# Optimization experiments

Measured on AMD Instinct MI355X. Metric: run time of the kernel, lower is better.

## Reference

```python
import jax, jax.numpy as jnp
import numpy as np

K = 7  # local_kernel_size


def conv2d(x, w, b, pad):
    # x: [B,C,H,W], w: [O,I,kh,kw]
    y = jax.lax.conv_general_dilated(
        x, w, window_strides=(1, 1), padding=[(pad, pad), (pad, pad)],
        dimension_numbers=("NCHW", "OIHW", "NCHW"))
    return y + b[None, :, None, None]


def kernel_normalize(kernel, k):
    # kernel: [B, k*k, H, W]; zero-mean over tap dim, then add 1/(k*k)
    km = jnp.mean(kernel, axis=1, keepdims=True)
    return kernel - km + 1.0 / (k * k)


def local_conv_feat(img, kernel, k):
    # Fused dynamic local conv: avoids materializing [B,C,k*k,H,W].
    # Tap order matches F.unfold row-major (dy, dx).
    B, C, H, W = img.shape
    pad = (k - 1) // 2
    imgp = jnp.pad(img, ((0, 0), (0, 0), (pad, pad), (pad, pad)))
    out = jnp.zeros_like(img)
    for dy in range(k):
        for dx in range(k):
            idx = dy * k + dx
            out = out + imgp[:, :, dy:dy + H, dx:dx + W] * kernel[:, idx:idx + 1]
    return out


def setup_inputs() -> dict:
    key = jax.random.key(0)
    ks = jax.random.split(key, 14)
    B, C, H, W = 4, 64, 128, 128
    w = lambda k, shape: jax.random.normal(k, shape, jnp.float32) * 0.05
    return {
        "x": jax.random.normal(ks[0], (B, C, H, W), jnp.float32),
        "kernel_features": jax.random.normal(ks[1], (B, C, H, W), jnp.float32),
        # feature_path: two 3x3 convs
        "fw1": w(ks[2], (C, C, 3, 3)), "fb1": jnp.zeros((C,), jnp.float32),
        "fw2": w(ks[3], (C, C, 3, 3)), "fb2": jnp.zeros((C,), jnp.float32),
        # multiplicative_path: two 3x3 convs
        "mw1": w(ks[4], (C, C, 3, 3)), "mb1": jnp.zeros((C,), jnp.float32),
        "mw2": w(ks[5], (C, C, 3, 3)), "mb2": jnp.zeros((C,), jnp.float32),
        # local_filter_path: two 1x1 convs, last outputs k*k channels
        "lw1": w(ks[6], (C, C, 1, 1)), "lb1": jnp.zeros((C,), jnp.float32),
        "lw2": w(ks[7], (K * K, C, 1, 1)), "lb2": jnp.zeros((K * K,), jnp.float32),
    }


def reference(x, kernel_features, fw1, fb1, fw2, fb2, mw1, mb1, mw2, mb2, lw1, lb1, lw2, lb2):
    # feature_path: ReLU -> conv3x3 -> ReLU -> conv3x3
    fp = conv2d(jax.nn.relu(conv2d(jax.nn.relu(x), fw1, fb1, 1)), fw2, fb2, 1)
    # multiplicative_path: conv3x3 -> ReLU -> conv3x3
    mp = conv2d(jax.nn.relu(conv2d(kernel_features, mw1, mb1, 1)), mw2, mb2, 1)
    # local_filter_path: conv1x1 -> ReLU -> conv1x1 (-> k*k channels)
    lp = conv2d(jax.nn.relu(conv2d(kernel_features, lw1, lb1, 0)), lw2, lb2, 0)
    lp = kernel_normalize(lp, K)
    feat = fp * mp
    filtered = local_conv_feat(feat, lp, K)
    return x + filtered
```

## Files before the change

### kernel.cpp

```cpp
#include <hip/hip_runtime.h>
#include <hip/hip_bf16.h>

#define Cc 64
#define Hc 128
#define Wc 128
#define HWc (Hc * Wc)
#define Bc 4

typedef __attribute__((ext_vector_type(8))) short short8;
typedef __attribute__((ext_vector_type(4))) float float4v;

static __device__ __forceinline__ unsigned short f2bu(float f) {
    __hip_bfloat16 h = __float2bfloat16(f);
    return *(unsigned short*)&h;
}

__global__ __launch_bounds__(256) void cvt_both_k(
    const float* __restrict__ x, const float* __restrict__ kf,
    unsigned short* __restrict__ xb, unsigned short* __restrict__ kfb)
{
    const int bid = blockIdx.x;
    const bool isx = bid < 256;
    const float* src = isx ? x : kf;
    unsigned short* dst = isx ? xb : kfb;
    const int px = (isx ? bid : bid - 256) * 256 + threadIdx.x;
    const int b  = px >> 14;
    const int hw = px & 16383;
    const float* s = src + (size_t)b * Cc * HWc + hw;
    unsigned short* d = dst + (size_t)px * Cc;

#pragma unroll
    for (int c8 = 0; c8 < 8; ++c8) {
        unsigned int pk[4];
#pragma unroll
        for (int jp = 0; jp < 4; ++jp) {
            float v0 = s[(size_t)(c8 * 8 + jp * 2 + 0) * HWc];
            float v1 = s[(size_t)(c8 * 8 + jp * 2 + 1) * HWc];
            if (isx) { v0 = fmaxf(v0, 0.f); v1 = fmaxf(v1, 0.f); }
            pk[jp] = (unsigned int)f2bu(v0) | ((unsigned int)f2bu(v1) << 16);
        }
        *(uint4*)(d + c8 * 8) = make_uint4(pk[0], pk[1], pk[2], pk[3]);
    }
}

__global__ __launch_bounds__(256) void wpack_all_k(
    const float* __restrict__ fw1, const float* __restrict__ fw2,
    const float* __restrict__ mw1, const float* __restrict__ mw2,
    const float* __restrict__ lw1, const float* __restrict__ lw2,
    unsigned short* __restrict__ wbase)
{
    const int bid = blockIdx.x;
    const int tid = threadIdx.x;
    if (bid < 72) {
        const int which = bid / 18;
        const float* w = (which == 0) ? fw1 : (which == 1) ? fw2 : (which == 2) ? mw1 : mw2;
        unsigned short* wb = wbase + (size_t)which * 36864;
        const int g = (bid % 18) * 256 + tid;
        if (g >= 4608) return;
        const int lane = g & 63;
        const int smt  = g >> 6;
        const int s    = smt >> 2;
        const int mt   = smt & 3;
        const int co   = mt * 16 + (lane & 15);
        const int kb   = s * 32 + (lane >> 4) * 8;
        unsigned int pk[4];
#pragma unroll
        for (int jp = 0; jp < 4; ++jp) {
            int k0 = kb + jp * 2, k1 = k0 + 1;
            float v0 = w[((size_t)co * Cc + (k0 & 63)) * 9 + (k0 >> 6)];
            float v1 = w[((size_t)co * Cc + (k1 & 63)) * 9 + (k1 >> 6)];
            pk[jp] = (unsigned int)f2bu(v0) | ((unsigned int)f2bu(v1) << 16);
        }
        *(uint4*)(wb + (size_t)g * 8) = make_uint4(pk[0], pk[1], pk[2], pk[3]);
    } else {
        const int which = (bid - 72) >> 1;
        const float* w = which ? lw2 : lw1;
        const int Cout = which ? 49 : 64;
        unsigned short* wb = wbase + 4 * 36864 + (size_t)which * 4096;
        const int g = ((bid - 72) & 1) * 256 + tid;
        const int lane = g & 63;
        const int smt  = g >> 6;
        const int s    = smt >> 2;
        const int mt   = smt & 3;
        const int co   = mt * 16 + (lane & 15);
        const int kb   = s * 32 + (lane >> 4) * 8;
        unsigned int pk[4];
#pragma unroll
        for (int jp = 0; jp < 4; ++jp) {
            int k0 = kb + jp * 2, k1 = k0 + 1;
            float v0 = (co < Cout) ? w[(size_t)co * Cc + k0] : 0.f;
            float v1 = (co < Cout) ? w[(size_t)co * Cc + k1] : 0.f;
            pk[jp] = (unsigned int)f2bu(v0) | ((unsigned int)f2bu(v1) << 16);
        }
        *(uint4*)(wb + (size_t)g * 8) = make_uint4(pk[0], pk[1], pk[2], pk[3]);
    }
}

#define STAGE_TILE(INPTR)                                                     \
    for (int u = tid; u < 264; u += 256) {                                    \
        const int r_  = u / 66;                                               \
        const int c_  = u - r_ * 66;                                          \
        const int gh_ = h0 - 1 + r_;                                          \
        const int gw_ = w0 - 1 + c_;                                          \
        const bool ok_ = ((unsigned)gh_ < (unsigned)Hc) && ((unsigned)gw_ < (unsigned)Wc); \
        const unsigned short* src_ =                                          \
            (INPTR) + (((size_t)b * Hc + (ok_ ? gh_ : 0)) * Wc + (ok_ ? gw_ : 0)) * Cc; \
        const int sw_ = u & 7;                                                \
        _Pragma("unroll")                                                     \
        for (int ch_ = 0; ch_ < 8; ++ch_) {                                   \
            uint4 v_ = ok_ ? *(const uint4*)(src_ + ch_ * 8) : make_uint4(0, 0, 0, 0); \
            *(uint4*)&s_b[u * 64 + ((ch_ ^ sw_) << 3)] = v_;                  \
        }                                                                     \
    }

#define LOAD_A(W, s, m) (*(const short8*)((W) + (size_t)(s) * 2048 + (size_t)(m) * 512))
#define LOAD_B(s, nt) ({                                                      \
        const int tap_ = (s) >> 1;                                            \
        const int qb_  = rowb[tap_ / 3] + tap_ % 3;                           \
        const int ch0_ = ((s) & 1) * 4 + quad;                                \
        *(const short8*)&s_b[(qb_ + (nt) * 16) * 64 + ((ch0_ ^ (qb_ & 7)) << 3)]; })

#define CONV_GEMM(APTR, ACC)                                                  \
    {                                                                         \
        short8 a_cur[2], b_cur[4];                                            \
        _Pragma("unroll")                                                     \
        for (int m = 0; m < 2; ++m) a_cur[m] = LOAD_A(APTR, 0, m);            \
        _Pragma("unroll")                                                     \
        for (int nt = 0; nt < 4; ++nt) b_cur[nt] = LOAD_B(0, nt);             \
        _Pragma("unroll")                                                     \
        for (int s = 0; s < 18; ++s) {                                        \
            short8 a_nxt[2], b_nxt[4];                                        \
            if (s < 17) {                                                     \
                _Pragma("unroll")                                             \
                for (int m = 0; m < 2; ++m) a_nxt[m] = LOAD_A(APTR, s + 1, m);\
                _Pragma("unroll")                                             \
                for (int nt = 0; nt < 4; ++nt) b_nxt[nt] = LOAD_B(s + 1, nt); \
            }                                                                 \
            _Pragma("unroll")                                                 \
            for (int nt = 0; nt < 4; ++nt)                                    \
                _Pragma("unroll")                                             \
                for (int m = 0; m < 2; ++m)                                   \
                    ACC[m][nt] = __builtin_amdgcn_mfma_f32_16x16x32_bf16(     \
                        a_cur[m], b_cur[nt], ACC[m][nt], 0, 0, 0);            \
            if (s < 17) {                                                     \
                _Pragma("unroll")                                             \
                for (int m = 0; m < 2; ++m) a_cur[m] = a_nxt[m];              \
                _Pragma("unroll")                                             \
                for (int nt = 0; nt < 4; ++nt) b_cur[nt] = b_nxt[nt];         \
            }                                                                 \
        }                                                                     \
    }

__global__ __launch_bounds__(256) void conv1_dual_k(
    const unsigned short* __restrict__ in0,
    const unsigned short* __restrict__ in1,
    const unsigned short* __restrict__ wfrag0,
    const unsigned short* __restrict__ wfrag1,
    const float* __restrict__ bias0,
    const float* __restrict__ bias1,
    unsigned short* __restrict__ out0,
    unsigned short* __restrict__ out1)
{
    __shared__ unsigned short s_b[264 * 64];

    const int tid  = threadIdx.x;
    const int lane = tid & 63;
    const int wv   = tid >> 6;
    const int w0   = blockIdx.x * 64;
    const int h0   = blockIdx.y * 2;
    const int zz   = blockIdx.z;
    const int b    = zz & 3;
    const bool sel = zz >> 2;

    const unsigned short* in    = sel ? in1 : in0;
    const unsigned short* wfrag = sel ? wfrag1 : wfrag0;
    const float*          bias  = sel ? bias1 : bias0;
    unsigned short*       out   = sel ? out1 : out0;

    STAGE_TILE(in);
    __syncthreads();

    const int rowsel = wv >> 1;
    const int cohalf = wv & 1;
    const int quad   = lane >> 4;
    const int n15    = lane & 15;
    const unsigned short* aptr = wfrag + (((size_t)(cohalf * 2) * 64 + lane) << 3);

    int rowb[3];
#pragma unroll
    for (int ky = 0; ky < 3; ++ky) rowb[ky] = (rowsel + ky) * 66 + n15;

    float4v acc[2][4];
#pragma unroll
    for (int m = 0; m < 2; ++m)
#pragma unroll
        for (int nt = 0; nt < 4; ++nt) acc[m][nt] = (float4v){0.f, 0.f, 0.f, 0.f};

    CONV_GEMM(aptr, acc);

    const int h = h0 + rowsel;
#pragma unroll
    for (int m = 0; m < 2; ++m) {
        const int mt  = cohalf * 2 + m;
        const int co0 = mt * 16 + quad * 4;
        float4 bv = *(const float4*)&bias[co0];
#pragma unroll
        for (int nt = 0; nt < 4; ++nt) {
            const size_t pix = ((size_t)b * Hc + h) * Wc + w0 + nt * 16 + n15;
            ushort4 pk;
            pk.x = f2bu(fmaxf(acc[m][nt][0] + bv.x, 0.f));
            pk.y = f2bu(fmaxf(acc[m][nt][1] + bv.y, 0.f));
            pk.z = f2bu(fmaxf(acc[m][nt][2] + bv.z, 0.f));
            pk.w = f2bu(fmaxf(acc[m][nt][3] + bv.w, 0.f));
            *(ushort4*)&out[pix * Cc + co0] = pk;
        }
    }
}

__global__ __launch_bounds__(256) void conv2_fused_k(
    const unsigned short* __restrict__ t1f,
    const unsigned short* __restrict__ t1m,
    const unsigned short* __restrict__ wf,
    const unsigned short* __restrict__ wm,
    const float* __restrict__ bf,
    const float* __restrict__ bm,
    float* __restrict__ feat)
{
    __shared__ unsigned short s_b[264 * 64];

    const int tid  = threadIdx.x;
    const int lane = tid & 63;
    const int wv   = tid >> 6;
    const int w0   = blockIdx.x * 64;
    const int h0   = blockIdx.y * 2;
    const int b    = blockIdx.z;

    const int rowsel = wv >> 1;
    const int cohalf = wv & 1;
    const int quad   = lane >> 4;
    const int n15    = lane & 15;

    int rowb[3];
#pragma unroll
    for (int ky = 0; ky < 3; ++ky) rowb[ky] = (rowsel + ky) * 66 + n15;

    STAGE_TILE(t1f);
    __syncthreads();

    float4v acc[2][4];
#pragma unroll
    for (int m = 0; m < 2; ++m)
#pragma unroll
        for (int nt = 0; nt < 4; ++nt) acc[m][nt] = (float4v){0.f, 0.f, 0.f, 0.f};

    {
        const unsigned short* aptr = wf + (((size_t)(cohalf * 2) * 64 + lane) << 3);
        CONV_GEMM(aptr, acc);
    }

    unsigned int fpk[2][4][2];
#pragma unroll
    for (int m = 0; m < 2; ++m) {
        const int mt  = cohalf * 2 + m;
        const int co0 = mt * 16 + quad * 4;
        float4 bv = *(const float4*)&bf[co0];
#pragma unroll
        for (int nt = 0; nt < 4; ++nt) {
            fpk[m][nt][0] = (unsigned int)f2bu(acc[m][nt][0] + bv.x)
                          | ((unsigned int)f2bu(acc[m][nt][1] + bv.y) << 16);
            fpk[m][nt][1] = (unsigned int)f2bu(acc[m][nt][2] + bv.z)
                          | ((unsigned int)f2bu(acc[m][nt][3] + bv.w) << 16);
        }
    }

    __syncthreads();

    STAGE_TILE(t1m);
    __syncthreads();

#pragma unroll
    for (int m = 0; m < 2; ++m)
#pragma unroll
        for (int nt = 0; nt < 4; ++nt) acc[m][nt] = (float4v){0.f, 0.f, 0.f, 0.f};

    {
        const unsigned short* aptr = wm + (((size_t)(cohalf * 2) * 64 + lane) << 3);
        CONV_GEMM(aptr, acc);
    }

    const int h = h0 + rowsel;
#pragma unroll
    for (int m = 0; m < 2; ++m) {
        const int mt  = cohalf * 2 + m;
        const int co0 = mt * 16 + quad * 4;
        float4 bv = *(const float4*)&bm[co0];
#pragma unroll
        for (int nt = 0; nt < 4; ++nt) {
            float v[4] = {acc[m][nt][0] + bv.x, acc[m][nt][1] + bv.y,
                          acc[m][nt][2] + bv.z, acc[m][nt][3] + bv.w};
            v[0] *= __uint_as_float((fpk[m][nt][0] & 0xffffu) << 16);
            v[1] *= __uint_as_float(fpk[m][nt][0] & 0xffff0000u);
            v[2] *= __uint_as_float((fpk[m][nt][1] & 0xffffu) << 16);
            v[3] *= __uint_as_float(fpk[m][nt][1] & 0xffff0000u);
#pragma unroll
            for (int r = 0; r < 4; ++r)
                feat[((size_t)b * Cc + co0 + r) * HWc + (size_t)h * Wc + w0 + nt * 16 + n15] = v[r];
        }
    }
}

__global__ __launch_bounds__(256) void lp_fused_k(
    const unsigned short* __restrict__ in,
    const unsigned short* __restrict__ w1,
    const float* __restrict__ b1,
    const unsigned short* __restrict__ w2,
    const float* __restrict__ b2,
    float* __restrict__ out)
{
    __shared__ unsigned short s_t[4 * 1024];

    const int tid  = threadIdx.x;
    const int lane = tid & 63;
    const int wv   = tid >> 6;
    const int quad = lane >> 4;
    const int p    = lane & 15;
    const size_t pix = (size_t)blockIdx.x * 64 + wv * 16 + p;
    unsigned short* st = &s_t[wv * 1024];

    float4v acc1[4];
#pragma unroll
    for (int mt = 0; mt < 4; ++mt) acc1[mt] = (float4v){0.f, 0.f, 0.f, 0.f};
#pragma unroll
    for (int s = 0; s < 2; ++s) {
        short8 bfr = *(const short8*)&in[pix * Cc + s * 32 + quad * 8];
#pragma unroll
        for (int mt = 0; mt < 4; ++mt) {
            short8 afr = *(const short8*)&w1[(size_t)(((s * 4 + mt) << 6) + lane) << 3];
            acc1[mt] = __builtin_amdgcn_mfma_f32_16x16x32_bf16(afr, bfr, acc1[mt], 0, 0, 0);
        }
    }

#pragma unroll
    for (int mt = 0; mt < 4; ++mt) {
        const int co0 = mt * 16 + quad * 4;
        float4 bv = *(const float4*)&b1[co0];
        ushort4 pk;
        pk.x = f2bu(fmaxf(acc1[mt][0] + bv.x, 0.f));
        pk.y = f2bu(fmaxf(acc1[mt][1] + bv.y, 0.f));
        pk.z = f2bu(fmaxf(acc1[mt][2] + bv.z, 0.f));
        pk.w = f2bu(fmaxf(acc1[mt][3] + bv.w, 0.f));
        const int cg = co0 >> 3;
        *(ushort4*)&st[p * 64 + ((cg ^ (p & 7)) << 3) + (quad & 1) * 4] = pk;
    }
    __syncthreads();

    float4v acc2[4];
#pragma unroll
    for (int mt = 0; mt < 4; ++mt) acc2[mt] = (float4v){0.f, 0.f, 0.f, 0.f};
#pragma unroll
    for (int s = 0; s < 2; ++s) {
        const int cg = s * 4 + quad;
        short8 bfr = *(const short8*)&st[p * 64 + ((cg ^ (p & 7)) << 3)];
#pragma unroll
        for (int mt = 0; mt < 4; ++mt) {
            short8 afr = *(const short8*)&w2[(size_t)(((s * 4 + mt) << 6) + lane) << 3];
            acc2[mt] = __builtin_amdgcn_mfma_f32_16x16x32_bf16(afr, bfr, acc2[mt], 0, 0, 0);
        }
    }

    float v[4][4];
    float partial = 0.f;
#pragma unroll
    for (int mt = 0; mt < 4; ++mt) {
#pragma unroll
        for (int r = 0; r < 4; ++r) {
            const int tap = mt * 16 + quad * 4 + r;
            float val = (tap < 49) ? (acc2[mt][r] + b2[tap]) : 0.f;
            v[mt][r] = val;
            partial += val;
        }
    }
    partial += __shfl_xor(partial, 16, 64);
    partial += __shfl_xor(partial, 32, 64);
    const float m = partial * (1.f / 49.f) - (1.f / 49.f);

    const int b  = (int)(pix >> 14);
    const int hw = (int)(pix & 16383);
#pragma unroll
    for (int mt = 0; mt < 4; ++mt) {
#pragma unroll
        for (int r = 0; r < 4; ++r) {
            const int tap = mt * 16 + quad * 4 + r;
            if (tap < 49)
                out[((size_t)b * 49 + tap) * HWc + hw] = v[mt][r] - m;
        }
    }
}

__global__ __launch_bounds__(256) void local_conv_v2(
    const float* __restrict__ x, const float* __restrict__ feat,
    const float* __restrict__ lp, float* __restrict__ out)
{
    const int tid = threadIdx.x;
    const int w4  = (tid & 31) * 4;
    const int ro  = tid >> 5;
    const int h   = blockIdx.y * 8 + ro;
    const int c0  = blockIdx.x * 4;
    const int b   = blockIdx.z;

    float msk[12];
#pragma unroll
    for (int e = 0; e < 12; ++e) {
        int gw = w4 - 4 + e;
        msk[e] = ((unsigned)gw < (unsigned)Wc) ? 1.f : 0.f;
    }

    float acc[4][4];
#pragma unroll
    for (int ch = 0; ch < 4; ++ch)
#pragma unroll
        for (int p = 0; p < 4; ++p) acc[ch][p] = 0.f;

    const float* lpb = lp + (size_t)b * 49 * HWc + (size_t)h * Wc + w4;
    const float* fb  = feat + ((size_t)b * Cc + c0) * HWc;

#pragma unroll
    for (int dy = 0; dy < 7; ++dy) {
        const int gh = h + dy - 3;
        if ((unsigned)gh >= (unsigned)Hc) continue;

        float4 lp4[7];
#pragma unroll
        for (int dx = 0; dx < 7; ++dx)
            lp4[dx] = *(const float4*)&lpb[(size_t)(dy * 7 + dx) * HWc];

        const float* frow = fb + (size_t)gh * Wc + w4;
#pragma unroll
        for (int ch = 0; ch < 4; ++ch) {
            const float* fr = frow + (size_t)ch * HWc;
            float4 a  = *(const float4*)(fr - 4);
            float4 bq = *(const float4*)(fr);
            float4 cq = *(const float4*)(fr + 4);
            float f[12];
            f[0]  = a.x;            f[1]  = a.y * msk[1];
            f[2]  = a.z * msk[2];   f[3]  = a.w * msk[3];
            f[4]  = bq.x;           f[5]  = bq.y;
            f[6]  = bq.z;           f[7]  = bq.w;
            f[8]  = cq.x * msk[8];  f[9]  = cq.y * msk[9];
            f[10] = cq.z * msk[10]; f[11] = cq.w;
#pragma unroll
            for (int dx = 0; dx < 7; ++dx) {
                const float* lpv = (const float*)&lp4[dx];
#pragma unroll
                for (int p = 0; p < 4; ++p)
                    acc[ch][p] = fmaf(f[p + dx + 1], lpv[p], acc[ch][p]);
            }
        }
    }

#pragma unroll
    for (int ch = 0; ch < 4; ++ch) {
        const size_t idx = ((size_t)b * Cc + c0 + ch) * HWc + (size_t)h * Wc + w4;
        float4 xv = *(const float4*)&x[idx];
        float4 r  = {acc[ch][0] + xv.x, acc[ch][1] + xv.y,
                     acc[ch][2] + xv.z, acc[ch][3] + xv.w};
        *(float4*)&out[idx] = r;
    }
}

extern "C" void kernel_launch(void* const* d_in, const int* in_sizes, int n_in,
                              void* d_out, int out_size, void* d_ws, size_t ws_size,
                              hipStream_t stream)
{
    const float* x   = (const float*)d_in[0];
    const float* kf  = (const float*)d_in[1];
    const float* fw1 = (const float*)d_in[2];
    const float* fb1 = (const float*)d_in[3];
    const float* fw2 = (const float*)d_in[4];
    const float* fb2 = (const float*)d_in[5];
    const float* mw1 = (const float*)d_in[6];
    const float* mb1 = (const float*)d_in[7];
    const float* mw2 = (const float*)d_in[8];
    const float* mb2 = (const float*)d_in[9];
    const float* lw1 = (const float*)d_in[10];
    const float* lb1 = (const float*)d_in[11];
    const float* lw2 = (const float*)d_in[12];
    const float* lb2 = (const float*)d_in[13];

    float* out = (float*)d_out;
    char*  ws  = (char*)d_ws;

    const size_t NBH = (size_t)Bc * HWc * Cc * 2;
    const size_t NBF = (size_t)Bc * Cc * HWc * 4;
    const size_t LPB = (size_t)Bc * 49 * HWc * 4;

    unsigned short* t1f   = (unsigned short*)(ws);
    unsigned short* t1m   = (unsigned short*)(ws + NBH);
    float*          feat  = (float*)(ws + 2 * NBH);
    float*          lpb   = (float*)(ws + 2 * NBH + NBF);
    unsigned short* xb    = (unsigned short*)(ws + 2 * NBH + NBF + LPB);
    unsigned short* kfb   = (unsigned short*)((char*)xb + NBH);
    unsigned short* wbase = (unsigned short*)((char*)kfb + NBH);
    unsigned short* wb1   = wbase;
    unsigned short* wb2   = wbase + 36864;
    unsigned short* wb3   = wbase + 2 * 36864;
    unsigned short* wb4   = wbase + 3 * 36864;
    unsigned short* wl1   = wbase + 4 * 36864;
    unsigned short* wl2   = wbase + 4 * 36864 + 4096;

    dim3 blk(256);
    dim3 gm2(Wc / 64, Hc / 2, Bc * 2);
    dim3 gm (Wc / 64, Hc / 2, Bc);
    dim3 gp (Bc * HWc / 64);
    dim3 glc(Cc / 4, Hc / 8, Bc);

    cvt_both_k<<<dim3(512), blk, 0, stream>>>(x, kf, xb, kfb);
    wpack_all_k<<<dim3(76), blk, 0, stream>>>(fw1, fw2, mw1, mw2, lw1, lw2, wbase);

    conv1_dual_k<<<gm2, blk, 0, stream>>>(xb, kfb, wb1, wb3, fb1, mb1, t1f, t1m);

    conv2_fused_k<<<gm, blk, 0, stream>>>(t1f, t1m, wb2, wb4, fb2, mb2, feat);

    lp_fused_k<<<gp, blk, 0, stream>>>(kfb, wl1, lb1, wl2, lb2, lpb);

    local_conv_v2<<<glc, blk, 0, stream>>>(x, feat, lpb, out);
}
```

Baseline: 192.0 us.

## Stage conv tiles via global_load_lds DMA, double-buffer conv2 inputs, merge prep kernels

Replaces the register-staged halo tile loads in both conv kernels with direct global-to-LDS loads (global_load_lds), using a zeroed page for out-of-bounds pixels. conv2 now stages both input tiles up front into two LDS buffers, which removes the mid-kernel barrier and restage. The conversion and weight-packing kernels are merged into one launch. The cost is double the LDS in conv2, which may lower occupancy, plus an extra memset.

```diff
diff --git a/kernel.cpp b/kernel.cpp
--- a/kernel.cpp
+++ b/kernel.cpp
@@ -15,47 +15,50 @@
     return *(unsigned short*)&h;
 }
 
-__global__ __launch_bounds__(256) void cvt_both_k(
+static __device__ __forceinline__ void gl_lds16(const void* g, void* l) {
+    __builtin_amdgcn_global_load_lds(
+        (const __attribute__((address_space(1))) unsigned int*)g,
+        (__attribute__((address_space(3))) unsigned int*)l, 16, 0, 0);
+}
+
+__global__ __launch_bounds__(256) void prep_k(
     const float* __restrict__ x, const float* __restrict__ kf,
-    unsigned short* __restrict__ xb, unsigned short* __restrict__ kfb)
-{
-    const int bid = blockIdx.x;
-    const bool isx = bid < 256;
-    const float* src = isx ? x : kf;
-    unsigned short* dst = isx ? xb : kfb;
-    const int px = (isx ? bid : bid - 256) * 256 + threadIdx.x;
-    const int b  = px >> 14;
-    const int hw = px & 16383;
-    const float* s = src + (size_t)b * Cc * HWc + hw;
-    unsigned short* d = dst + (size_t)px * Cc;
-
-#pragma unroll
-    for (int c8 = 0; c8 < 8; ++c8) {
-        unsigned int pk[4];
-#pragma unroll
-        for (int jp = 0; jp < 4; ++jp) {
-            float v0 = s[(size_t)(c8 * 8 + jp * 2 + 0) * HWc];
-            float v1 = s[(size_t)(c8 * 8 + jp * 2 + 1) * HWc];
-            if (isx) { v0 = fmaxf(v0, 0.f); v1 = fmaxf(v1, 0.f); }
-            pk[jp] = (unsigned int)f2bu(v0) | ((unsigned int)f2bu(v1) << 16);
-        }
-        *(uint4*)(d + c8 * 8) = make_uint4(pk[0], pk[1], pk[2], pk[3]);
-    }
-}
-
-__global__ __launch_bounds__(256) void wpack_all_k(
     const float* __restrict__ fw1, const float* __restrict__ fw2,
     const float* __restrict__ mw1, const float* __restrict__ mw2,
     const float* __restrict__ lw1, const float* __restrict__ lw2,
+    unsigned short* __restrict__ xb, unsigned short* __restrict__ kfb,
     unsigned short* __restrict__ wbase)
 {
     const int bid = blockIdx.x;
     const int tid = threadIdx.x;
-    if (bid < 72) {
-        const int which = bid / 18;
+
+    if (bid < 512) {
+        const bool isx = bid < 256;
+        const float* src = isx ? x : kf;
+        unsigned short* dst = isx ? xb : kfb;
+        const int px = (isx ? bid : bid - 256) * 256 + tid;
+        const int b  = px >> 14;
+        const int hw = px & 16383;
+        const float* s = src + (size_t)b * Cc * HWc + hw;
+        unsigned short* d = dst + (size_t)px * Cc;
+#pragma unroll
+        for (int c8 = 0; c8 < 8; ++c8) {
+            unsigned int pk[4];
+#pragma unroll
+            for (int jp = 0; jp < 4; ++jp) {
+                float v0 = s[(size_t)(c8 * 8 + jp * 2 + 0) * HWc];
+                float v1 = s[(size_t)(c8 * 8 + jp * 2 + 1) * HWc];
+                if (isx) { v0 = fmaxf(v0, 0.f); v1 = fmaxf(v1, 0.f); }
+                pk[jp] = (unsigned int)f2bu(v0) | ((unsigned int)f2bu(v1) << 16);
+            }
+            *(uint4*)(d + c8 * 8) = make_uint4(pk[0], pk[1], pk[2], pk[3]);
+        }
+    } else if (bid < 584) {
+        const int wbid  = bid - 512;
+        const int which = wbid / 18;
         const float* w = (which == 0) ? fw1 : (which == 1) ? fw2 : (which == 2) ? mw1 : mw2;
         unsigned short* wb = wbase + (size_t)which * 36864;
-        const int g = (bid % 18) * 256 + tid;
+        const int g = (wbid % 18) * 256 + tid;
         if (g >= 4608) return;
         const int lane = g & 63;
         const int smt  = g >> 6;
@@ -73,11 +76,12 @@
         }
         *(uint4*)(wb + (size_t)g * 8) = make_uint4(pk[0], pk[1], pk[2], pk[3]);
     } else {
-        const int which = (bid - 72) >> 1;
+        const int wbid  = bid - 584;
+        const int which = wbid >> 1;
         const float* w = which ? lw2 : lw1;
         const int Cout = which ? 49 : 64;
         unsigned short* wb = wbase + 4 * 36864 + (size_t)which * 4096;
-        const int g = ((bid - 72) & 1) * 256 + tid;
+        const int g = (wbid & 1) * 256 + tid;
         const int lane = g & 63;
         const int smt  = g >> 6;
         const int s    = smt >> 2;
@@ -96,37 +100,36 @@
     }
 }
 
-#define STAGE_TILE(INPTR)                                                     \
-    for (int u = tid; u < 264; u += 256) {                                    \
-        const int r_  = u / 66;                                               \
-        const int c_  = u - r_ * 66;                                          \
+#define STAGE_DMA(INPTR, SBUF)                                                \
+    for (int k = wv; k < 33; k += 4) {                                        \
+        const int u_  = k * 8 + (lane >> 3);                                  \
+        const int j_  = lane & 7;                                             \
+        const int r_  = u_ / 66;                                              \
+        const int c_  = u_ - r_ * 66;                                         \
         const int gh_ = h0 - 1 + r_;                                          \
         const int gw_ = w0 - 1 + c_;                                          \
         const bool ok_ = ((unsigned)gh_ < (unsigned)Hc) && ((unsigned)gw_ < (unsigned)Wc); \
-        const unsigned short* src_ =                                          \
-            (INPTR) + (((size_t)b * Hc + (ok_ ? gh_ : 0)) * Wc + (ok_ ? gw_ : 0)) * Cc; \
-        const int sw_ = u & 7;                                                \
-        _Pragma("unroll")                                                     \
-        for (int ch_ = 0; ch_ < 8; ++ch_) {                                   \
-            uint4 v_ = ok_ ? *(const uint4*)(src_ + ch_ * 8) : make_uint4(0, 0, 0, 0); \
-            *(uint4*)&s_b[u * 64 + ((ch_ ^ sw_) << 3)] = v_;                  \
-        }                                                                     \
+        const int ch_ = j_ ^ (u_ & 7);                                        \
+        const unsigned short* g_ = ok_                                        \
+            ? (INPTR) + ((((size_t)b * Hc + gh_) * Wc + gw_) << 6) + (ch_ << 3) \
+            : zpage + (ch_ << 3);                                             \
+        gl_lds16(g_, &(SBUF)[k * 512]);                                       \
     }
 
 #define LOAD_A(W, s, m) (*(const short8*)((W) + (size_t)(s) * 2048 + (size_t)(m) * 512))
-#define LOAD_B(s, nt) ({                                                      \
+#define LOAD_B(SB, s, nt) ({                                                  \
         const int tap_ = (s) >> 1;                                            \
         const int qb_  = rowb[tap_ / 3] + tap_ % 3;                           \
         const int ch0_ = ((s) & 1) * 4 + quad;                                \
-        *(const short8*)&s_b[(qb_ + (nt) * 16) * 64 + ((ch0_ ^ (qb_ & 7)) << 3)]; })
-
-#define CONV_GEMM(APTR, ACC)                                                  \
+        *(const short8*)&(SB)[(qb_ + (nt) * 16) * 64 + ((ch0_ ^ (qb_ & 7)) << 3)]; })
+
+#define CONV_GEMM(APTR, ACC, SB)                                              \
     {                                                                         \
         short8 a_cur[2], b_cur[4];                                            \
         _Pragma("unroll")                                                     \
         for (int m = 0; m < 2; ++m) a_cur[m] = LOAD_A(APTR, 0, m);            \
         _Pragma("unroll")                                                     \
-        for (int nt = 0; nt < 4; ++nt) b_cur[nt] = LOAD_B(0, nt);             \
+        for (int nt = 0; nt < 4; ++nt) b_cur[nt] = LOAD_B(SB, 0, nt);         \
         _Pragma("unroll")                                                     \
         for (int s = 0; s < 18; ++s) {                                        \
             short8 a_nxt[2], b_nxt[4];                                        \
@@ -134,7 +137,7 @@
                 _Pragma("unroll")                                             \
                 for (int m = 0; m < 2; ++m) a_nxt[m] = LOAD_A(APTR, s + 1, m);\
                 _Pragma("unroll")                                             \
-                for (int nt = 0; nt < 4; ++nt) b_nxt[nt] = LOAD_B(s + 1, nt); \
+                for (int nt = 0; nt < 4; ++nt) b_nxt[nt] = LOAD_B(SB, s + 1, nt); \
             }                                                                 \
             _Pragma("unroll")                                                 \
             for (int nt = 0; nt < 4; ++nt)                                    \
@@ -158,6 +161,7 @@
     const unsigned short* __restrict__ wfrag1,
     const float* __restrict__ bias0,
     const float* __restrict__ bias1,
+    const unsigned short* __restrict__ zpage,
     unsigned short* __restrict__ out0,
     unsigned short* __restrict__ out1)
 {
@@ -177,7 +181,7 @@
     const float*          bias  = sel ? bias1 : bias0;
     unsigned short*       out   = sel ? out1 : out0;
 
-    STAGE_TILE(in);
+    STAGE_DMA(in, s_b);
     __syncthreads();
 
     const int rowsel = wv >> 1;
@@ -196,7 +200,7 @@
 #pragma unroll
         for (int nt = 0; nt < 4; ++nt) acc[m][nt] = (float4v){0.f, 0.f, 0.f, 0.f};
 
-    CONV_GEMM(aptr, acc);
+    CONV_GEMM(aptr, acc, s_b);
 
     const int h = h0 + rowsel;
 #pragma unroll
@@ -224,9 +228,10 @@
     const unsigned short* __restrict__ wm,
     const float* __restrict__ bf,
     const float* __restrict__ bm,
+    const unsigned short* __restrict__ zpage,
     float* __restrict__ feat)
 {
-    __shared__ unsigned short s_b[264 * 64];
+    __shared__ unsigned short s_b2[2][264 * 64];
 
     const int tid  = threadIdx.x;
     const int lane = tid & 63;
@@ -235,6 +240,10 @@
     const int h0   = blockIdx.y * 2;
     const int b    = blockIdx.z;
 
+    STAGE_DMA(t1f, s_b2[0]);
+    STAGE_DMA(t1m, s_b2[1]);
+    __syncthreads();
+
     const int rowsel = wv >> 1;
     const int cohalf = wv & 1;
     const int quad   = lane >> 4;
@@ -244,9 +253,6 @@
 #pragma unroll
     for (int ky = 0; ky < 3; ++ky) rowb[ky] = (rowsel + ky) * 66 + n15;
 
-    STAGE_TILE(t1f);
-    __syncthreads();
-
     float4v acc[2][4];
 #pragma unroll
     for (int m = 0; m < 2; ++m)
@@ -255,7 +261,7 @@
 
     {
         const unsigned short* aptr = wf + (((size_t)(cohalf * 2) * 64 + lane) << 3);
-        CONV_GEMM(aptr, acc);
+        CONV_GEMM(aptr, acc, s_b2[0]);
     }
 
     unsigned int fpk[2][4][2];
@@ -273,11 +279,6 @@
         }
     }
 
-    __syncthreads();
-
-    STAGE_TILE(t1m);
-    __syncthreads();
-
 #pragma unroll
     for (int m = 0; m < 2; ++m)
 #pragma unroll
@@ -285,7 +286,7 @@
 
     {
         const unsigned short* aptr = wm + (((size_t)(cohalf * 2) * 64 + lane) << 3);
-        CONV_GEMM(aptr, acc);
+        CONV_GEMM(aptr, acc, s_b2[1]);
     }
 
     const int h = h0 + rowsel;
@@ -493,6 +494,7 @@
     const size_t NBH = (size_t)Bc * HWc * Cc * 2;
     const size_t NBF = (size_t)Bc * Cc * HWc * 4;
     const size_t LPB = (size_t)Bc * 49 * HWc * 4;
+    const size_t WBA = (size_t)(4 * 36864 + 2 * 4096) * 2;
 
     unsigned short* t1f   = (unsigned short*)(ws);
     unsigned short* t1m   = (unsigned short*)(ws + NBH);
@@ -501,6 +503,7 @@
     unsigned short* xb    = (unsigned short*)(ws + 2 * NBH + NBF + LPB);
     unsigned short* kfb   = (unsigned short*)((char*)xb + NBH);
     unsigned short* wbase = (unsigned short*)((char*)kfb + NBH);
+    unsigned short* zpage = (unsigned short*)((char*)wbase + WBA);
     unsigned short* wb1   = wbase;
     unsigned short* wb2   = wbase + 36864;
     unsigned short* wb3   = wbase + 2 * 36864;
@@ -514,12 +517,14 @@
     dim3 gp (Bc * HWc / 64);
     dim3 glc(Cc / 4, Hc / 8, Bc);
 
-    cvt_both_k<<<dim3(512), blk, 0, stream>>>(x, kf, xb, kfb);
-    wpack_all_k<<<dim3(76), blk, 0, stream>>>(fw1, fw2, mw1, mw2, lw1, lw2, wbase);
-
-    conv1_dual_k<<<gm2, blk, 0, stream>>>(xb, kfb, wb1, wb3, fb1, mb1, t1f, t1m);
-
-    conv2_fused_k<<<gm, blk, 0, stream>>>(t1f, t1m, wb2, wb4, fb2, mb2, feat);
+    hipMemsetAsync(zpage, 0, 256, stream);
+
+    prep_k<<<dim3(588), blk, 0, stream>>>(x, kf, fw1, fw2, mw1, mw2, lw1, lw2,
+                                          xb, kfb, wbase);
+
+    conv1_dual_k<<<gm2, blk, 0, stream>>>(xb, kfb, wb1, wb3, fb1, mb1, zpage, t1f, t1m);
+
+    conv2_fused_k<<<gm, blk, 0, stream>>>(t1f, t1m, wb2, wb4, fb2, mb2, zpage, feat);
 
     lp_fused_k<<<gp, blk, 0, stream>>>(kfb, wl1, lb1, wl2, lb2, lpb);
 
```

Result: faster. 180.2 us (-6.1%).
